# Optimization experiments

Measured on AMD Instinct MI355X. Metric: run time of the kernel, lower is better.

The kernel has to match this reference:

```python
import jax, jax.numpy as jnp
import numpy as np

MODEL_DIM = 1024
NUM_HEADS = 16
CHUNK_LEN = 2048
HEAD_DIM = MODEL_DIM // NUM_HEADS


def setup_inputs() -> dict:
    key = jax.random.key(0)
    ks = jax.random.split(key, 11)
    s = 1.0 / np.sqrt(MODEL_DIM)
    inp = {
        "Q": jax.random.normal(ks[0], (CHUNK_LEN, MODEL_DIM), dtype=jnp.float32),
        "K": jax.random.normal(ks[1], (CHUNK_LEN, MODEL_DIM), dtype=jnp.float32),
        "V": jax.random.normal(ks[2], (CHUNK_LEN, MODEL_DIM), dtype=jnp.float32),
        "Wq": jax.random.normal(ks[3], (MODEL_DIM, MODEL_DIM), dtype=jnp.float32) * s,
        "bq": jax.random.normal(ks[4], (MODEL_DIM,), dtype=jnp.float32) * s,
        "Wk": jax.random.normal(ks[5], (MODEL_DIM, MODEL_DIM), dtype=jnp.float32) * s,
        "bk": jax.random.normal(ks[6], (MODEL_DIM,), dtype=jnp.float32) * s,
        "Wv": jax.random.normal(ks[7], (MODEL_DIM, MODEL_DIM), dtype=jnp.float32) * s,
        "bv": jax.random.normal(ks[8], (MODEL_DIM,), dtype=jnp.float32) * s,
        "Wo": jax.random.normal(ks[9], (MODEL_DIM, MODEL_DIM), dtype=jnp.float32) * s,
        "bo": jax.random.normal(ks[10], (MODEL_DIM,), dtype=jnp.float32) * s,
    }
    return inp


def reference(Q, K, V, Wq, bq, Wk, bk, Wv, bv, Wo, bo):
    S = CHUNK_LEN
    # Linear projections (equinox Linear: y = W @ x + b, vmapped over tokens)
    q = Q @ Wq.T + bq  # [S, D]
    k = K @ Wk.T + bk
    v = V @ Wv.T + bv
    # split heads -> [H, S, hd]
    q = q.reshape(S, NUM_HEADS, HEAD_DIM).transpose(1, 0, 2)
    k = k.reshape(S, NUM_HEADS, HEAD_DIM).transpose(1, 0, 2)
    v = v.reshape(S, NUM_HEADS, HEAD_DIM).transpose(1, 0, 2)
    # scaled dot-product attention with causal mask
    scores = jnp.einsum("hqd,hkd->hqk", q, k) / jnp.sqrt(
        jnp.asarray(HEAD_DIM, dtype=q.dtype)
    )  # [H, S, S]
    causal = jnp.tril(jnp.ones((S, S), dtype=bool))
    scores = jnp.where(causal, scores, -jnp.inf)
    probs = jax.nn.softmax(scores, axis=-1)
    attn = jnp.einsum("hqk,hkd->hqd", probs, v)  # [H, S, hd]
    # combine heads -> [S, D], output projection
    out = attn.transpose(1, 0, 2).reshape(S, MODEL_DIM)
    return out @ Wo.T + bo
```

## Files before the change

### kernel.cpp

```cpp
#include <hip/hip_runtime.h>
#include <hip/hip_bf16.h>
#include <stdint.h>

#define S_LEN  2048
#define DMODEL 1024
#define NHEADS 16
#define HDIM   64
#define CHUNK  7
#define NCHUNK 46
#define LOG2E  1.4426950408889634f

typedef __attribute__((ext_vector_type(8))) _Float16 half8;
typedef __attribute__((ext_vector_type(4))) _Float16 half4;
typedef __attribute__((ext_vector_type(4))) float    f32x4;

struct AttnMap { int base[17]; };

struct CvtArgs {
    const float* src[7];
    _Float16*    dst[7];
    int          n[7];
};

__global__ __launch_bounds__(256) void cvt_kernel(CvtArgs a) {
    const int z = blockIdx.z;
    const float* __restrict__ src = a.src[z];
    _Float16* __restrict__ dst = a.dst[z];
    const int n = a.n[z];
    const int stride = gridDim.x * blockDim.x * 8;
    for (int i = (blockIdx.x * blockDim.x + threadIdx.x) * 8; i < n; i += stride) {
        float4 v0 = *(const float4*)(src + i);
        float4 v1 = *(const float4*)(src + i + 4);
        half8 o;
        o[0] = (_Float16)v0.x; o[1] = (_Float16)v0.y;
        o[2] = (_Float16)v0.z; o[3] = (_Float16)v0.w;
        o[4] = (_Float16)v1.x; o[5] = (_Float16)v1.y;
        o[6] = (_Float16)v1.z; o[7] = (_Float16)v1.w;
        *(half8*)(dst + i) = o;
    }
}

__device__ __forceinline__ void gload16(const _Float16* g, _Float16* l) {
    __builtin_amdgcn_global_load_lds(
        (__attribute__((address_space(1))) void*)const_cast<_Float16*>(g),
        (__attribute__((address_space(3))) void*)l, 16, 0, 0);
}

template<int BM, typename OT>
__device__ __forceinline__ void gemm_body(
    const _Float16* __restrict__ A,
    const _Float16* __restrict__ W,
    const float*    __restrict__ bias,
    OT* __restrict__ C, float scale, int bx, int by)
{
    constexpr int FI = BM / 32;
    __shared__ _Float16 As[2][BM * 64];
    __shared__ _Float16 Bs[2][64 * 64];
    const int tid  = threadIdx.x;
    const int lane = tid & 63, wid = tid >> 6;
    const int row0 = by * BM;
    const int col0 = bx * 64;
    const int wr = wid >> 1, wc = wid & 1;
    const int lr = lane & 15, lg = lane >> 4;
    const int sl = lane & 7;

    f32x4 acc[FI][2];
#pragma unroll
    for (int i = 0; i < FI; i++)
#pragma unroll
        for (int j = 0; j < 2; j++) acc[i][j] = (f32x4)(0.0f);

    auto stage = [&](int b, int k0) {
#pragma unroll
        for (int r = 0; r < BM / 32; r++) {
            const int base = r * 256 + wid * 64;
            const int row  = (base + lane) >> 3;
            gload16(A + (size_t)(row0 + row) * DMODEL + k0 + ((sl ^ (row & 7)) * 8),
                    &As[b][(size_t)base * 8]);
        }
#pragma unroll
        for (int r = 0; r < 2; r++) {
            const int base = r * 256 + wid * 64;
            const int row  = (base + lane) >> 3;
            gload16(W + (size_t)(col0 + row) * DMODEL + k0 + ((sl ^ (row & 7)) * 8),
                    &Bs[b][(size_t)base * 8]);
        }
    };

    stage(0, 0);
    __syncthreads();
    int cur = 0;
    for (int t = 0; t < DMODEL / 64; t++) {
        if (t + 1 < DMODEL / 64) stage(cur ^ 1, (t + 1) * 64);
#pragma unroll
        for (int ks = 0; ks < 2; ks++) {
            half8 af[FI], bf[2];
#pragma unroll
            for (int i = 0; i < FI; i++)
                af[i] = *(const half8*)(&As[cur][(wr * (BM / 2) + i * 16 + lr) * 64 + (((ks * 4 + lg) ^ (lr & 7)) * 8)]);
#pragma unroll
            for (int j = 0; j < 2; j++)
                bf[j] = *(const half8*)(&Bs[cur][(wc * 32 + j * 16 + lr) * 64 + (((ks * 4 + lg) ^ (lr & 7)) * 8)]);
            __builtin_amdgcn_s_setprio(1);
#pragma unroll
            for (int i = 0; i < FI; i++)
#pragma unroll
                for (int j = 0; j < 2; j++)
                    acc[i][j] = __builtin_amdgcn_mfma_f32_16x16x32_f16(af[i], bf[j], acc[i][j], 0, 0, 0);
            __builtin_amdgcn_s_setprio(0);
        }
        __syncthreads();
        cur ^= 1;
    }
#pragma unroll
    for (int i = 0; i < FI; i++)
#pragma unroll
        for (int j = 0; j < 2; j++) {
            const int row = row0 + wr * (BM / 2) + i * 16 + lg * 4;
            const int col = col0 + wc * 32 + j * 16 + lr;
            const float b = bias[col];
#pragma unroll
            for (int rj = 0; rj < 4; rj++) {
                float v = (acc[i][j][rj] + b) * scale;
                if constexpr (sizeof(OT) == 2)
                    C[(size_t)(row + rj) * DMODEL + col] = (OT)(_Float16)v;
                else
                    C[(size_t)(row + rj) * DMODEL + col] = v;
            }
        }
}

struct QKVArgs {
    const _Float16* A[3];
    const _Float16* W[3];
    const float*    bias[3];
    _Float16*       C[3];
    float           scale[3];
};

__global__ __launch_bounds__(256) void gemm_qkv(QKVArgs a) {
    const int nper = (int)gridDim.x >> 3;
    const int sid  = ((int)blockIdx.x & 7) * nper + ((int)blockIdx.x >> 3);
    const int z  = sid >> 8;
    const int r  = sid & 255;
    const int by = r >> 4, bx = r & 15;
    gemm_body<128, _Float16>(a.A[z], a.W[z], a.bias[z], a.C[z], a.scale[z], bx, by);
}

__global__ __launch_bounds__(256) void gemm_out_k(const _Float16* __restrict__ A,
                                                  const _Float16* __restrict__ W,
                                                  const float* __restrict__ bias,
                                                  float* __restrict__ C) {
    const int nper = (int)gridDim.x >> 3;
    const int sid  = ((int)blockIdx.x & 7) * nper + ((int)blockIdx.x >> 3);
    const int by = sid >> 4, bx = sid & 15;
    gemm_body<64, float>(A, W, bias, C, 1.0f, bx, by);
}

__global__ __launch_bounds__(256) void transpose_v(const _Float16* __restrict__ v,
                                                   _Float16* __restrict__ Vt) {
    __shared__ _Float16 t[64][72];
    const int s0 = blockIdx.x * 64;
    const int h  = blockIdx.y;
    const int tid = threadIdx.x;
#pragma unroll
    for (int r = 0; r < 2; r++) {
        const int g = r * 256 + tid;
        const int sr = g >> 3, c8 = (g & 7) * 8;
        *(half8*)(&t[sr][c8]) = *(const half8*)(v + (size_t)(s0 + sr) * DMODEL + h * HDIM + c8);
    }
    __syncthreads();
#pragma unroll
    for (int r = 0; r < 2; r++) {
        const int g = r * 256 + tid;
        const int d = g >> 3, c8 = (g & 7) * 8;
        half8 o;
#pragma unroll
        for (int j = 0; j < 8; j++) o[j] = t[c8 + j][d];
        *(half8*)(Vt + (size_t)(h * HDIM + d) * S_LEN + s0 + c8) = o;
    }
}

__global__ __launch_bounds__(512, 6) void attn_kernel(
    const _Float16* __restrict__ q,
    const _Float16* __restrict__ k,
    const _Float16* __restrict__ Vt,
    _Float16* __restrict__ Opart,
    float2* __restrict__ ml,
    AttnMap map)
{
    __shared__ _Float16 Kl[2][64 * 64];
    __shared__ _Float16 Vl[2][64 * 64];
    __shared__ _Float16 P[8][16][72];
    const int tid = threadIdx.x, lane = tid & 63, wid = tid >> 6;
    const int x = NCHUNK - 1 - (int)blockIdx.x;
    const int h = blockIdx.y;
    int qt = 0;
    while (map.base[qt + 1] <= x) qt++;
    const int c  = x - map.base[qt];
    const int q0 = qt * 128 + wid * 16;
    const int lr = lane & 15, lg = lane >> 4;
    const int srcb = lg * 20;

    const int r8 = lane >> 3, sl = lane & 7;
    const int ssw = (sl ^ r8) * 8;

    half8 qf[2];
#pragma unroll
    for (int ds = 0; ds < 2; ds++)
        qf[ds] = *(const half8*)(q + (size_t)(q0 + lr) * DMODEL + h * HDIM + ds * 32 + lg * 8);

    float m = -1e30f, lsum = 0.0f;
    f32x4 od[4];
#pragma unroll
    for (int dt = 0; dt < 4; dt++) od[dt] = (f32x4)(0.0f);

    const int T2 = 2 * (qt + 1);
    const int t0 = c * CHUNK;
    const int t1 = (T2 < t0 + CHUNK) ? T2 : (t0 + CHUNK);

    auto stage = [&](int b, int t) {
        const int kb = t * 64;
        gload16(k + (size_t)(kb + wid * 8 + r8) * DMODEL + h * HDIM + ssw,
                &Kl[b][wid * 8 * 64]);
        gload16(Vt + (size_t)(h * HDIM + wid * 8 + r8) * S_LEN + kb + ssw,
                &Vl[b][wid * 8 * 64]);
    };

    int cur = 0;
    stage(0, t0);
    __syncthreads();

    for (int t = t0; t < t1; t++) {
        if (t + 1 < t1) stage(cur ^ 1, t + 1);
        const int k0 = t * 64;
        f32x4 sc[4];
#pragma unroll
        for (int kt = 0; kt < 4; kt++) sc[kt] = (f32x4)(0.0f);
        __builtin_amdgcn_s_setprio(1);
#pragma unroll
        for (int kt = 0; kt < 4; kt++)
#pragma unroll
            for (int ds = 0; ds < 2; ds++) {
                half8 kf = *(const half8*)(&Kl[cur][(kt * 16 + lr) * 64 + (((ds * 4 + lg) ^ (lr & 7)) * 8)]);
                sc[kt] = __builtin_amdgcn_mfma_f32_16x16x32_f16(kf, qf[ds], sc[kt], 0, 0, 0);
            }
        __builtin_amdgcn_s_setprio(0);
        if (k0 + 63 > q0) {
            const int qrow = q0 + lr;
#pragma unroll
            for (int kt = 0; kt < 4; kt++) {
                const int kb2 = k0 + kt * 16 + lg * 4;
#pragma unroll
                for (int r = 0; r < 4; r++)
                    if (kb2 + r > qrow) sc[kt][r] = -1e30f;
            }
        }
        float mk[4];
#pragma unroll
        for (int kt = 0; kt < 4; kt++)
            mk[kt] = fmaxf(fmaxf(sc[kt][0], sc[kt][1]), fmaxf(sc[kt][2], sc[kt][3]));
        float vmax = fmaxf(fmaxf(mk[0], mk[1]), fmaxf(mk[2], mk[3]));
        vmax = fmaxf(vmax, __shfl_xor(vmax, 16));
        vmax = fmaxf(vmax, __shfl_xor(vmax, 32));
        if (!__all(vmax <= m + 8.0f)) {
            const float mnew = fmaxf(m, vmax);
            const float sfac = exp2f(m - mnew);
            m = mnew;
            lsum *= sfac;
            float sf[4];
#pragma unroll
            for (int r = 0; r < 4; r++) sf[r] = __shfl(sfac, srcb + r);
#pragma unroll
            for (int dt = 0; dt < 4; dt++)
#pragma unroll
                for (int r = 0; r < 4; r++) od[dt][r] *= sf[r];
        }
        float ps[4];
#pragma unroll
        for (int kt = 0; kt < 4; kt++) {
            float p0 = exp2f(sc[kt][0] - m), p1 = exp2f(sc[kt][1] - m);
            float p2 = exp2f(sc[kt][2] - m), p3 = exp2f(sc[kt][3] - m);
            sc[kt][0] = p0; sc[kt][1] = p1; sc[kt][2] = p2; sc[kt][3] = p3;
            ps[kt] = (p0 + p1) + (p2 + p3);
        }
        float psum = (ps[0] + ps[1]) + (ps[2] + ps[3]);
        psum += __shfl_xor(psum, 16);
        psum += __shfl_xor(psum, 32);
        lsum += psum;
#pragma unroll
        for (int kt = 0; kt < 4; kt++) {
            half4 ph;
#pragma unroll
            for (int r = 0; r < 4; r++) ph[r] = (_Float16)sc[kt][r];
            *(half4*)(&P[wid][lr][kt * 16 + lg * 4]) = ph;
        }
        __builtin_amdgcn_s_setprio(1);
#pragma unroll
        for (int ks = 0; ks < 2; ks++) {
            half8 pa = *(const half8*)(&P[wid][lr][ks * 32 + lg * 8]);
#pragma unroll
            for (int dt = 0; dt < 4; dt++) {
                half8 vb = *(const half8*)(&Vl[cur][(dt * 16 + lr) * 64 + (((ks * 4 + lg) ^ (lr & 7)) * 8)]);
                od[dt] = __builtin_amdgcn_mfma_f32_16x16x32_f16(pa, vb, od[dt], 0, 0, 0);
            }
        }
        __builtin_amdgcn_s_setprio(0);
        __syncthreads();
        cur ^= 1;
    }

    const float inv = 1.0f / lsum;
    float invb[4];
#pragma unroll
    for (int r = 0; r < 4; r++) invb[r] = __shfl(inv, srcb + r);
    _Float16* Ob = Opart + ((size_t)h * NCHUNK + x) * 128 * 64;
#pragma unroll
    for (int dt = 0; dt < 4; dt++)
#pragma unroll
        for (int r = 0; r < 4; r++)
            Ob[(size_t)(wid * 16 + lg * 4 + r) * 64 + dt * 16 + lr] = (_Float16)(od[dt][r] * invb[r]);
    if (lane < 16) {
        float2 v; v.x = m; v.y = lsum;
        ml[((size_t)h * NCHUNK + x) * 128 + wid * 16 + lr] = v;
    }
}

__global__ __launch_bounds__(256) void combine_kernel(
    const _Float16* __restrict__ Opart, const float2* __restrict__ ml,
    _Float16* __restrict__ at, AttnMap map)
{
    const int idx = blockIdx.x * 256 + threadIdx.x;
    const int qrow = idx >> 7;
    const int c8 = (idx & 127) * 8;
    const int h = c8 >> 6, d = c8 & 63;
    const int qt = qrow >> 7;
    const int cb = map.base[qt];
    const int nc = map.base[qt + 1] - cb;
    const int lrow = qrow & 127;

    float M = -1e30f, denom = 0.0f;
    float acc[8];
#pragma unroll
    for (int j = 0; j < 8; j++) acc[j] = 0.0f;
    for (int cc = 0; cc < nc; cc++) {
        const size_t ci = (size_t)h * NCHUNK + cb + cc;
        const float2 mlv = ml[ci * 128 + lrow];
        half8 ov = *(const half8*)(Opart + (ci * 128 + lrow) * 64 + d);
        if (mlv.x > M) {
            const float r = exp2f(M - mlv.x);
            denom = denom * r + mlv.y;
#pragma unroll
            for (int j = 0; j < 8; j++) acc[j] = acc[j] * r + (float)ov[j] * mlv.y;
            M = mlv.x;
        } else {
            const float w = exp2f(mlv.x - M) * mlv.y;
            denom += w;
#pragma unroll
            for (int j = 0; j < 8; j++) acc[j] += (float)ov[j] * w;
        }
    }
    const float inv = 1.0f / denom;
    half8 o;
#pragma unroll
    for (int j = 0; j < 8; j++) o[j] = (_Float16)(acc[j] * inv);
    *(half8*)(at + (size_t)qrow * DMODEL + c8) = o;
}

extern "C" void kernel_launch(void* const* d_in, const int* in_sizes, int n_in,
                              void* d_out, int out_size, void* d_ws, size_t ws_size,
                              hipStream_t stream) {
    const float* Q  = (const float*)d_in[0];
    const float* K  = (const float*)d_in[1];
    const float* V  = (const float*)d_in[2];
    const float* Wq = (const float*)d_in[3];
    const float* bq = (const float*)d_in[4];
    const float* Wk = (const float*)d_in[5];
    const float* bk = (const float*)d_in[6];
    const float* Wv = (const float*)d_in[7];
    const float* bv = (const float*)d_in[8];
    const float* Wo = (const float*)d_in[9];
    const float* bo = (const float*)d_in[10];

    char* w = (char*)d_ws;
    const size_t MB = 1 << 20;
    _Float16* Qh  = (_Float16*)(w + 0 * MB);
    _Float16* Kh  = (_Float16*)(w + 4 * MB);
    _Float16* Vh  = (_Float16*)(w + 8 * MB);
    _Float16* Wqh = (_Float16*)(w + 12 * MB);
    _Float16* Wkh = (_Float16*)(w + 14 * MB);
    _Float16* Wvh = (_Float16*)(w + 16 * MB);
    _Float16* vh  = (_Float16*)(w + 18 * MB);
    _Float16* Woh = (_Float16*)(w + 22 * MB);
    _Float16* qh  = (_Float16*)(w + 24 * MB);
    _Float16* kh  = (_Float16*)(w + 28 * MB);
    _Float16* Vt    = (_Float16*)(w + 0 * MB);
    _Float16* Opart = (_Float16*)(w + 4 * MB);
    float2*   ml    = (float2*)(w + 4 * MB + (size_t)NHEADS * NCHUNK * 128 * 64 * 2);
    _Float16* at    = (_Float16*)(w + 18 * MB);

    const size_t SD = (size_t)S_LEN * DMODEL;
    const size_t WD = (size_t)DMODEL * DMODEL;

    CvtArgs ca;
    ca.src[0] = Q;  ca.dst[0] = Qh;  ca.n[0] = (int)SD;
    ca.src[1] = K;  ca.dst[1] = Kh;  ca.n[1] = (int)SD;
    ca.src[2] = V;  ca.dst[2] = Vh;  ca.n[2] = (int)SD;
    ca.src[3] = Wq; ca.dst[3] = Wqh; ca.n[3] = (int)WD;
    ca.src[4] = Wk; ca.dst[4] = Wkh; ca.n[4] = (int)WD;
    ca.src[5] = Wv; ca.dst[5] = Wvh; ca.n[5] = (int)WD;
    ca.src[6] = Wo; ca.dst[6] = Woh; ca.n[6] = (int)WD;
    cvt_kernel<<<dim3(1024, 1, 7), 256, 0, stream>>>(ca);

    QKVArgs ga;
    ga.A[0] = Qh; ga.W[0] = Wqh; ga.bias[0] = bq; ga.C[0] = qh; ga.scale[0] = 0.125f * LOG2E;
    ga.A[1] = Kh; ga.W[1] = Wkh; ga.bias[1] = bk; ga.C[1] = kh; ga.scale[1] = 1.0f;
    ga.A[2] = Vh; ga.W[2] = Wvh; ga.bias[2] = bv; ga.C[2] = vh; ga.scale[2] = 1.0f;
    gemm_qkv<<<dim3(768), 256, 0, stream>>>(ga);

    transpose_v<<<dim3(32, 16), 256, 0, stream>>>(vh, Vt);

    AttnMap map;
    map.base[0] = 0;
    for (int qt = 0; qt < 16; qt++)
        map.base[qt + 1] = map.base[qt] + (2 * (qt + 1) + CHUNK - 1) / CHUNK;

    attn_kernel<<<dim3(NCHUNK, NHEADS), 512, 0, stream>>>(qh, kh, Vt, Opart, ml, map);
    combine_kernel<<<dim3(1024), 256, 0, stream>>>(Opart, ml, at, map);
    gemm_out_k<<<dim3(512), 256, 0, stream>>>(at, Woh, bo, (float*)d_out);
}
```

Before: 83.70 us.

## Fuse V transpose into QKV GEMM epilogue and double attention query tile

The V projection now writes its output directly in transposed layout from the GEMM epilogue, which removes the separate transpose kernel and its extra round trip through memory. The attention kernel processes 32 query rows per wave instead of 16, with 256-row query tiles and key/value chunks of 5. This reuses each loaded K/V tile across twice as many queries and reduces the partial results the combine step must merge. The cost is more registers per wave, a lower occupancy hint (4 instead of 6), fewer attention blocks, and uncoalesced strided half4 stores in the transposed epilogue. The workspace layout and the convert launch grid are also changed.

```diff
diff --git a/kernel.cpp b/kernel.cpp
--- a/kernel.cpp
+++ b/kernel.cpp
@@ -6,15 +6,15 @@
 #define DMODEL 1024
 #define NHEADS 16
 #define HDIM   64
-#define CHUNK  7
-#define NCHUNK 46
+#define CHUNK  5
+#define NCHUNK 32
 #define LOG2E  1.4426950408889634f
 
 typedef __attribute__((ext_vector_type(8))) _Float16 half8;
 typedef __attribute__((ext_vector_type(4))) _Float16 half4;
 typedef __attribute__((ext_vector_type(4))) float    f32x4;
 
-struct AttnMap { int base[17]; };
+struct AttnMap { int base[9]; };
 
 struct CvtArgs {
     const float* src[7];
@@ -51,7 +51,7 @@
     const _Float16* __restrict__ A,
     const _Float16* __restrict__ W,
     const float*    __restrict__ bias,
-    OT* __restrict__ C, float scale, int bx, int by)
+    OT* __restrict__ C, float scale, int bx, int by, bool trans)
 {
     constexpr int FI = BM / 32;
     __shared__ _Float16 As[2][BM * 64];
@@ -119,13 +119,20 @@
             const int row = row0 + wr * (BM / 2) + i * 16 + lg * 4;
             const int col = col0 + wc * 32 + j * 16 + lr;
             const float b = bias[col];
-#pragma unroll
-            for (int rj = 0; rj < 4; rj++) {
-                float v = (acc[i][j][rj] + b) * scale;
-                if constexpr (sizeof(OT) == 2)
-                    C[(size_t)(row + rj) * DMODEL + col] = (OT)(_Float16)v;
-                else
-                    C[(size_t)(row + rj) * DMODEL + col] = v;
+            if (trans) {
+                half4 h;
+#pragma unroll
+                for (int rj = 0; rj < 4; rj++) h[rj] = (_Float16)((acc[i][j][rj] + b) * scale);
+                *(half4*)((_Float16*)C + (size_t)col * S_LEN + row) = h;
+            } else {
+#pragma unroll
+                for (int rj = 0; rj < 4; rj++) {
+                    float v = (acc[i][j][rj] + b) * scale;
+                    if constexpr (sizeof(OT) == 2)
+                        C[(size_t)(row + rj) * DMODEL + col] = (OT)(_Float16)v;
+                    else
+                        C[(size_t)(row + rj) * DMODEL + col] = v;
+                }
             }
         }
 }
@@ -144,7 +151,7 @@
     const int z  = sid >> 8;
     const int r  = sid & 255;
     const int by = r >> 4, bx = r & 15;
-    gemm_body<128, _Float16>(a.A[z], a.W[z], a.bias[z], a.C[z], a.scale[z], bx, by);
+    gemm_body<128, _Float16>(a.A[z], a.W[z], a.bias[z], a.C[z], a.scale[z], bx, by, z == 2);
 }
 
 __global__ __launch_bounds__(256) void gemm_out_k(const _Float16* __restrict__ A,
@@ -154,34 +161,10 @@
     const int nper = (int)gridDim.x >> 3;
     const int sid  = ((int)blockIdx.x & 7) * nper + ((int)blockIdx.x >> 3);
     const int by = sid >> 4, bx = sid & 15;
-    gemm_body<64, float>(A, W, bias, C, 1.0f, bx, by);
-}
-
-__global__ __launch_bounds__(256) void transpose_v(const _Float16* __restrict__ v,
-                                                   _Float16* __restrict__ Vt) {
-    __shared__ _Float16 t[64][72];
-    const int s0 = blockIdx.x * 64;
-    const int h  = blockIdx.y;
-    const int tid = threadIdx.x;
-#pragma unroll
-    for (int r = 0; r < 2; r++) {
-        const int g = r * 256 + tid;
-        const int sr = g >> 3, c8 = (g & 7) * 8;
-        *(half8*)(&t[sr][c8]) = *(const half8*)(v + (size_t)(s0 + sr) * DMODEL + h * HDIM + c8);
-    }
-    __syncthreads();
-#pragma unroll
-    for (int r = 0; r < 2; r++) {
-        const int g = r * 256 + tid;
-        const int d = g >> 3, c8 = (g & 7) * 8;
-        half8 o;
-#pragma unroll
-        for (int j = 0; j < 8; j++) o[j] = t[c8 + j][d];
-        *(half8*)(Vt + (size_t)(h * HDIM + d) * S_LEN + s0 + c8) = o;
-    }
-}
-
-__global__ __launch_bounds__(512, 6) void attn_kernel(
+    gemm_body<64, float>(A, W, bias, C, 1.0f, bx, by, false);
+}
+
+__global__ __launch_bounds__(512, 4) void attn_kernel(
     const _Float16* __restrict__ q,
     const _Float16* __restrict__ k,
     const _Float16* __restrict__ Vt,
@@ -191,33 +174,37 @@
 {
     __shared__ _Float16 Kl[2][64 * 64];
     __shared__ _Float16 Vl[2][64 * 64];
-    __shared__ _Float16 P[8][16][72];
+    __shared__ _Float16 P[8][32][72];
     const int tid = threadIdx.x, lane = tid & 63, wid = tid >> 6;
     const int x = NCHUNK - 1 - (int)blockIdx.x;
     const int h = blockIdx.y;
     int qt = 0;
     while (map.base[qt + 1] <= x) qt++;
     const int c  = x - map.base[qt];
-    const int q0 = qt * 128 + wid * 16;
+    const int q0 = qt * 256 + wid * 32;
     const int lr = lane & 15, lg = lane >> 4;
     const int srcb = lg * 20;
 
     const int r8 = lane >> 3, sl = lane & 7;
     const int ssw = (sl ^ r8) * 8;
 
-    half8 qf[2];
-#pragma unroll
-    for (int ds = 0; ds < 2; ds++)
-        qf[ds] = *(const half8*)(q + (size_t)(q0 + lr) * DMODEL + h * HDIM + ds * 32 + lg * 8);
-
-    float m = -1e30f, lsum = 0.0f;
-    f32x4 od[4];
-#pragma unroll
-    for (int dt = 0; dt < 4; dt++) od[dt] = (f32x4)(0.0f);
-
-    const int T2 = 2 * (qt + 1);
+    half8 qf[2][2];
+#pragma unroll
+    for (int qs = 0; qs < 2; qs++)
+#pragma unroll
+        for (int ds = 0; ds < 2; ds++)
+            qf[qs][ds] = *(const half8*)(q + (size_t)(q0 + qs * 16 + lr) * DMODEL + h * HDIM + ds * 32 + lg * 8);
+
+    float m[2] = {-1e30f, -1e30f}, lsum[2] = {0.0f, 0.0f};
+    f32x4 od[2][4];
+#pragma unroll
+    for (int qs = 0; qs < 2; qs++)
+#pragma unroll
+        for (int dt = 0; dt < 4; dt++) od[qs][dt] = (f32x4)(0.0f);
+
+    const int T4 = 4 * (qt + 1);
     const int t0 = c * CHUNK;
-    const int t1 = (T2 < t0 + CHUNK) ? T2 : (t0 + CHUNK);
+    const int t1 = (T4 < t0 + CHUNK) ? T4 : (t0 + CHUNK);
 
     auto stage = [&](int b, int t) {
         const int kb = t * 64;
@@ -234,75 +221,94 @@
     for (int t = t0; t < t1; t++) {
         if (t + 1 < t1) stage(cur ^ 1, t + 1);
         const int k0 = t * 64;
-        f32x4 sc[4];
-#pragma unroll
-        for (int kt = 0; kt < 4; kt++) sc[kt] = (f32x4)(0.0f);
+        f32x4 sc[2][4];
+#pragma unroll
+        for (int qs = 0; qs < 2; qs++)
+#pragma unroll
+            for (int kt = 0; kt < 4; kt++) sc[qs][kt] = (f32x4)(0.0f);
         __builtin_amdgcn_s_setprio(1);
 #pragma unroll
         for (int kt = 0; kt < 4; kt++)
 #pragma unroll
             for (int ds = 0; ds < 2; ds++) {
                 half8 kf = *(const half8*)(&Kl[cur][(kt * 16 + lr) * 64 + (((ds * 4 + lg) ^ (lr & 7)) * 8)]);
-                sc[kt] = __builtin_amdgcn_mfma_f32_16x16x32_f16(kf, qf[ds], sc[kt], 0, 0, 0);
+                sc[0][kt] = __builtin_amdgcn_mfma_f32_16x16x32_f16(kf, qf[0][ds], sc[0][kt], 0, 0, 0);
+                sc[1][kt] = __builtin_amdgcn_mfma_f32_16x16x32_f16(kf, qf[1][ds], sc[1][kt], 0, 0, 0);
             }
         __builtin_amdgcn_s_setprio(0);
         if (k0 + 63 > q0) {
-            const int qrow = q0 + lr;
+#pragma unroll
+            for (int qs = 0; qs < 2; qs++) {
+                const int qrow = q0 + qs * 16 + lr;
+#pragma unroll
+                for (int kt = 0; kt < 4; kt++) {
+                    const int kb2 = k0 + kt * 16 + lg * 4;
+#pragma unroll
+                    for (int r = 0; r < 4; r++)
+                        if (kb2 + r > qrow) sc[qs][kt][r] = -1e30f;
+                }
+            }
+        }
+        float vmax[2];
+#pragma unroll
+        for (int qs = 0; qs < 2; qs++) {
+            float mk[4];
+#pragma unroll
+            for (int kt = 0; kt < 4; kt++)
+                mk[kt] = fmaxf(fmaxf(sc[qs][kt][0], sc[qs][kt][1]), fmaxf(sc[qs][kt][2], sc[qs][kt][3]));
+            float v = fmaxf(fmaxf(mk[0], mk[1]), fmaxf(mk[2], mk[3]));
+            v = fmaxf(v, __shfl_xor(v, 16));
+            v = fmaxf(v, __shfl_xor(v, 32));
+            vmax[qs] = v;
+        }
+        if (!__all(vmax[0] <= m[0] + 8.0f && vmax[1] <= m[1] + 8.0f)) {
+#pragma unroll
+            for (int qs = 0; qs < 2; qs++) {
+                const float mnew = fmaxf(m[qs], vmax[qs]);
+                const float sfac = exp2f(m[qs] - mnew);
+                m[qs] = mnew;
+                lsum[qs] *= sfac;
+                float sf[4];
+#pragma unroll
+                for (int r = 0; r < 4; r++) sf[r] = __shfl(sfac, srcb + r);
+#pragma unroll
+                for (int dt = 0; dt < 4; dt++)
+#pragma unroll
+                    for (int r = 0; r < 4; r++) od[qs][dt][r] *= sf[r];
+            }
+        }
+#pragma unroll
+        for (int qs = 0; qs < 2; qs++) {
+            float ps[4];
 #pragma unroll
             for (int kt = 0; kt < 4; kt++) {
-                const int kb2 = k0 + kt * 16 + lg * 4;
-#pragma unroll
-                for (int r = 0; r < 4; r++)
-                    if (kb2 + r > qrow) sc[kt][r] = -1e30f;
-            }
-        }
-        float mk[4];
-#pragma unroll
-        for (int kt = 0; kt < 4; kt++)
-            mk[kt] = fmaxf(fmaxf(sc[kt][0], sc[kt][1]), fmaxf(sc[kt][2], sc[kt][3]));
-        float vmax = fmaxf(fmaxf(mk[0], mk[1]), fmaxf(mk[2], mk[3]));
-        vmax = fmaxf(vmax, __shfl_xor(vmax, 16));
-        vmax = fmaxf(vmax, __shfl_xor(vmax, 32));
-        if (!__all(vmax <= m + 8.0f)) {
-            const float mnew = fmaxf(m, vmax);
-            const float sfac = exp2f(m - mnew);
-            m = mnew;
-            lsum *= sfac;
-            float sf[4];
-#pragma unroll
-            for (int r = 0; r < 4; r++) sf[r] = __shfl(sfac, srcb + r);
-#pragma unroll
-            for (int dt = 0; dt < 4; dt++)
-#pragma unroll
-                for (int r = 0; r < 4; r++) od[dt][r] *= sf[r];
-        }
-        float ps[4];
-#pragma unroll
-        for (int kt = 0; kt < 4; kt++) {
-            float p0 = exp2f(sc[kt][0] - m), p1 = exp2f(sc[kt][1] - m);
-            float p2 = exp2f(sc[kt][2] - m), p3 = exp2f(sc[kt][3] - m);
-            sc[kt][0] = p0; sc[kt][1] = p1; sc[kt][2] = p2; sc[kt][3] = p3;
-            ps[kt] = (p0 + p1) + (p2 + p3);
-        }
-        float psum = (ps[0] + ps[1]) + (ps[2] + ps[3]);
-        psum += __shfl_xor(psum, 16);
-        psum += __shfl_xor(psum, 32);
-        lsum += psum;
-#pragma unroll
-        for (int kt = 0; kt < 4; kt++) {
-            half4 ph;
-#pragma unroll
-            for (int r = 0; r < 4; r++) ph[r] = (_Float16)sc[kt][r];
-            *(half4*)(&P[wid][lr][kt * 16 + lg * 4]) = ph;
+                float p0 = exp2f(sc[qs][kt][0] - m[qs]), p1 = exp2f(sc[qs][kt][1] - m[qs]);
+                float p2 = exp2f(sc[qs][kt][2] - m[qs]), p3 = exp2f(sc[qs][kt][3] - m[qs]);
+                sc[qs][kt][0] = p0; sc[qs][kt][1] = p1; sc[qs][kt][2] = p2; sc[qs][kt][3] = p3;
+                ps[kt] = (p0 + p1) + (p2 + p3);
+            }
+            float psum = (ps[0] + ps[1]) + (ps[2] + ps[3]);
+            psum += __shfl_xor(psum, 16);
+            psum += __shfl_xor(psum, 32);
+            lsum[qs] += psum;
+#pragma unroll
+            for (int kt = 0; kt < 4; kt++) {
+                half4 ph;
+#pragma unroll
+                for (int r = 0; r < 4; r++) ph[r] = (_Float16)sc[qs][kt][r];
+                *(half4*)(&P[wid][qs * 16 + lr][kt * 16 + lg * 4]) = ph;
+            }
         }
         __builtin_amdgcn_s_setprio(1);
 #pragma unroll
         for (int ks = 0; ks < 2; ks++) {
-            half8 pa = *(const half8*)(&P[wid][lr][ks * 32 + lg * 8]);
+            half8 pa0 = *(const half8*)(&P[wid][lr][ks * 32 + lg * 8]);
+            half8 pa1 = *(const half8*)(&P[wid][16 + lr][ks * 32 + lg * 8]);
 #pragma unroll
             for (int dt = 0; dt < 4; dt++) {
                 half8 vb = *(const half8*)(&Vl[cur][(dt * 16 + lr) * 64 + (((ks * 4 + lg) ^ (lr & 7)) * 8)]);
-                od[dt] = __builtin_amdgcn_mfma_f32_16x16x32_f16(pa, vb, od[dt], 0, 0, 0);
+                od[0][dt] = __builtin_amdgcn_mfma_f32_16x16x32_f16(pa0, vb, od[0][dt], 0, 0, 0);
+                od[1][dt] = __builtin_amdgcn_mfma_f32_16x16x32_f16(pa1, vb, od[1][dt], 0, 0, 0);
             }
         }
         __builtin_amdgcn_s_setprio(0);
@@ -310,19 +316,26 @@
         cur ^= 1;
     }
 
-    const float inv = 1.0f / lsum;
-    float invb[4];
-#pragma unroll
-    for (int r = 0; r < 4; r++) invb[r] = __shfl(inv, srcb + r);
-    _Float16* Ob = Opart + ((size_t)h * NCHUNK + x) * 128 * 64;
-#pragma unroll
-    for (int dt = 0; dt < 4; dt++)
-#pragma unroll
-        for (int r = 0; r < 4; r++)
-            Ob[(size_t)(wid * 16 + lg * 4 + r) * 64 + dt * 16 + lr] = (_Float16)(od[dt][r] * invb[r]);
+    _Float16* Ob = Opart + ((size_t)h * NCHUNK + x) * 256 * 64;
+#pragma unroll
+    for (int qs = 0; qs < 2; qs++) {
+        const float inv = 1.0f / lsum[qs];
+        float invb[4];
+#pragma unroll
+        for (int r = 0; r < 4; r++) invb[r] = __shfl(inv, srcb + r);
+#pragma unroll
+        for (int dt = 0; dt < 4; dt++)
+#pragma unroll
+            for (int r = 0; r < 4; r++)
+                Ob[(size_t)(wid * 32 + qs * 16 + lg * 4 + r) * 64 + dt * 16 + lr] =
+                    (_Float16)(od[qs][dt][r] * invb[r]);
+    }
     if (lane < 16) {
-        float2 v; v.x = m; v.y = lsum;
-        ml[((size_t)h * NCHUNK + x) * 128 + wid * 16 + lr] = v;
+#pragma unroll
+        for (int qs = 0; qs < 2; qs++) {
+            float2 v; v.x = m[qs]; v.y = lsum[qs];
+            ml[((size_t)h * NCHUNK + x) * 256 + wid * 32 + qs * 16 + lr] = v;
+        }
     }
 }
 
@@ -334,10 +347,10 @@
     const int qrow = idx >> 7;
     const int c8 = (idx & 127) * 8;
     const int h = c8 >> 6, d = c8 & 63;
-    const int qt = qrow >> 7;
+    const int qt = qrow >> 8;
     const int cb = map.base[qt];
     const int nc = map.base[qt + 1] - cb;
-    const int lrow = qrow & 127;
+    const int lrow = qrow & 255;
 
     float M = -1e30f, denom = 0.0f;
     float acc[8];
@@ -345,8 +358,8 @@
     for (int j = 0; j < 8; j++) acc[j] = 0.0f;
     for (int cc = 0; cc < nc; cc++) {
         const size_t ci = (size_t)h * NCHUNK + cb + cc;
-        const float2 mlv = ml[ci * 128 + lrow];
-        half8 ov = *(const half8*)(Opart + (ci * 128 + lrow) * 64 + d);
+        const float2 mlv = ml[ci * 256 + lrow];
+        half8 ov = *(const half8*)(Opart + (ci * 256 + lrow) * 64 + d);
         if (mlv.x > M) {
             const float r = exp2f(M - mlv.x);
             denom = denom * r + mlv.y;
@@ -384,20 +397,19 @@
 
     char* w = (char*)d_ws;
     const size_t MB = 1 << 20;
-    _Float16* Qh  = (_Float16*)(w + 0 * MB);
-    _Float16* Kh  = (_Float16*)(w + 4 * MB);
-    _Float16* Vh  = (_Float16*)(w + 8 * MB);
-    _Float16* Wqh = (_Float16*)(w + 12 * MB);
-    _Float16* Wkh = (_Float16*)(w + 14 * MB);
-    _Float16* Wvh = (_Float16*)(w + 16 * MB);
-    _Float16* vh  = (_Float16*)(w + 18 * MB);
-    _Float16* Woh = (_Float16*)(w + 22 * MB);
-    _Float16* qh  = (_Float16*)(w + 24 * MB);
-    _Float16* kh  = (_Float16*)(w + 28 * MB);
-    _Float16* Vt    = (_Float16*)(w + 0 * MB);
-    _Float16* Opart = (_Float16*)(w + 4 * MB);
-    float2*   ml    = (float2*)(w + 4 * MB + (size_t)NHEADS * NCHUNK * 128 * 64 * 2);
-    _Float16* at    = (_Float16*)(w + 18 * MB);
+    _Float16* Vt  = (_Float16*)(w + 0 * MB);
+    _Float16* qh  = (_Float16*)(w + 4 * MB);
+    _Float16* kh  = (_Float16*)(w + 8 * MB);
+    _Float16* Woh = (_Float16*)(w + 12 * MB);
+    _Float16* Qh  = (_Float16*)(w + 14 * MB);
+    _Float16* Kh  = (_Float16*)(w + 18 * MB);
+    _Float16* Vh  = (_Float16*)(w + 22 * MB);
+    _Float16* Wqh = (_Float16*)(w + 26 * MB);
+    _Float16* Wkh = (_Float16*)(w + 28 * MB);
+    _Float16* Wvh = (_Float16*)(w + 30 * MB);
+    _Float16* Opart = (_Float16*)(w + 14 * MB);
+    float2*   ml    = (float2*)(w + 30 * MB);
+    _Float16* at    = qh;
 
     const size_t SD = (size_t)S_LEN * DMODEL;
     const size_t WD = (size_t)DMODEL * DMODEL;
@@ -410,20 +422,18 @@
     ca.src[4] = Wk; ca.dst[4] = Wkh; ca.n[4] = (int)WD;
     ca.src[5] = Wv; ca.dst[5] = Wvh; ca.n[5] = (int)WD;
     ca.src[6] = Wo; ca.dst[6] = Woh; ca.n[6] = (int)WD;
-    cvt_kernel<<<dim3(1024, 1, 7), 256, 0, stream>>>(ca);
+    cvt_kernel<<<dim3(512, 1, 7), 256, 0, stream>>>(ca);
 
     QKVArgs ga;
     ga.A[0] = Qh; ga.W[0] = Wqh; ga.bias[0] = bq; ga.C[0] = qh; ga.scale[0] = 0.125f * LOG2E;
     ga.A[1] = Kh; ga.W[1] = Wkh; ga.bias[1] = bk; ga.C[1] = kh; ga.scale[1] = 1.0f;
-    ga.A[2] = Vh; ga.W[2] = Wvh; ga.bias[2] = bv; ga.C[2] = vh; ga.scale[2] = 1.0f;
+    ga.A[2] = Vh; ga.W[2] = Wvh; ga.bias[2] = bv; ga.C[2] = Vt; ga.scale[2] = 1.0f;
     gemm_qkv<<<dim3(768), 256, 0, stream>>>(ga);
-
-    transpose_v<<<dim3(32, 16), 256, 0, stream>>>(vh, Vt);
 
     AttnMap map;
     map.base[0] = 0;
-    for (int qt = 0; qt < 16; qt++)
-        map.base[qt + 1] = map.base[qt] + (2 * (qt + 1) + CHUNK - 1) / CHUNK;
+    for (int qt = 0; qt < 8; qt++)
+        map.base[qt + 1] = map.base[qt] + (4 * (qt + 1) + CHUNK - 1) / CHUNK;
 
     attn_kernel<<<dim3(NCHUNK, NHEADS), 512, 0, stream>>>(qh, kh, Vt, Opart, ml, map);
     combine_kernel<<<dim3(1024), 256, 0, stream>>>(Opart, ml, at, map);
```

Result: faster. 79.60 us, median of 3 (-4.9%).
